# Kernel tuning notes

Hardware: AMD Instinct MI355X
Metric: run time of the kernel (lower is better)

## Reference

```python
import jax, jax.numpy as jnp
import numpy as np

B, DIN, DOUT = 16, 64, 64
P1_, P2_, P3_ = 64, 32, 16
BN_EPS = 1e-5


def setup_inputs() -> dict:
    key = jax.random.key(0)
    ks = jax.random.split(key, 8)
    A = jax.random.normal(ks[0], (B, DIN, P1_, P2_, P3_), dtype=jnp.float32)
    ini_p = float(np.sqrt(3.0 / DOUT / DIN))
    ini_qk = float(np.sqrt(1.0 / DOUT / DIN))
    def uni(k, s):
        return jax.random.uniform(k, (DOUT, DIN), dtype=jnp.float32, minval=-s, maxval=s)
    return {
        "A": A,
        "P1": uni(ks[1], ini_p),
        "P2": uni(ks[2], ini_p),
        "P3": uni(ks[3], ini_p),
        "P4": uni(ks[4], ini_p),
        "q": uni(ks[5], ini_qk),
        "k": uni(ks[6], ini_qk),
        "gamma": jnp.ones((DOUT,), jnp.float32),
        "beta": jnp.zeros((DOUT,), jnp.float32),
        "permutation_size1": P1_,
        "permutation_size2": P2_,
        "permutation_size3": P3_,
        "BATCH_SIZE": B,
    }


def reference(A, P1, P2, P3, P4, q, k, gamma, beta,
              permutation_size1, permutation_size2, permutation_size3, BATCH_SIZE):
    b = BATCH_SIZE
    dout = P1.shape[0]
    p1, p2, p3 = permutation_size1, permutation_size2, permutation_size3
    # branch 1: full per-element channel mix  [B, dout, p1, p2, p3]
    A1 = jnp.einsum('oi,bixyz->boxyz', P1, A)
    # branch 2: mean over p3, project, broadcast over p3
    A2 = jnp.einsum('oi,bixy->boxy', P2, A.mean(-1))[..., None]
    # branch 3: mean over p2, project, broadcast over p2
    A3 = jnp.einsum('oi,bixz->boxz', P3, A.mean(-2))[:, :, :, None, :]
    # attention over p1 with flattened (p2*p3) as the contraction axis
    Q = jnp.einsum('oi,bixyz->boxyz', q, A).reshape(b, dout, p1, p2 * p3)
    K = jnp.einsum('oi,bixyz->boxyz', k, A).reshape(b, dout, p1, p2 * p3)
    Alpha = jnp.einsum('bcxm,bcym->bcxy', Q, K)  # [B, dout, p1, p1]
    Alpha_norm = jnp.abs(Alpha) / jnp.linalg.norm(Alpha, axis=3, keepdims=True)
    V = jnp.einsum('oi,bixyz->boxyz', P4, A).reshape(b, dout, p1, p2 * p3)
    Y = jnp.einsum('bcxy,bcym->bcxm', Alpha_norm, V).reshape(b, dout, p1, p2, p3)
    out = A1 + 0.1 * A2 + 0.1 * A3 + 0.1 * Y
    out = jax.nn.relu(out)
    # BatchNorm3d (training-mode batch statistics, biased variance)
    mean = out.mean(axis=(0, 2, 3, 4), keepdims=True)
    var = out.var(axis=(0, 2, 3, 4), keepdims=True)
    out = (out - mean) * jax.lax.rsqrt(var + BN_EPS)
    out = out * gamma[None, :, None, None, None] + beta[None, :, None, None, None]
    return out
```

## Files before the change

### kernel.cpp

```cpp
#include <hip/hip_runtime.h>

typedef __attribute__((ext_vector_type(8))) short short8;
typedef __attribute__((ext_vector_type(4))) float f32x4;
typedef __attribute__((ext_vector_type(8))) unsigned short u16x8;
typedef __attribute__((ext_vector_type(4))) unsigned short u16x4;
typedef __attribute__((ext_vector_type(4))) unsigned int u32x4;
typedef unsigned short u16;

#define DEVINL __device__ __forceinline__

DEVINL u16 f2bf(float f) {
  unsigned u = __builtin_bit_cast(unsigned, f);
  unsigned r = (u + 0x7fffu + ((u >> 16) & 1u)) >> 16;
  return (u16)r;
}
DEVINL float bf2f(u16 h) {
  unsigned u = ((unsigned)h) << 16;
  return __builtin_bit_cast(float, u);
}
DEVINL unsigned pk2(float a, float b) {
  return (unsigned)f2bf(a) | ((unsigned)f2bf(b) << 16);
}
DEVINL int swzc(int row, int chunk) { return chunk ^ ((row ^ (row >> 3)) & 7); }
DEVINL int tile_byte(int row, int chunk) { return row * 128 + swzc(row, chunk) * 16; }

__global__ void kw_convert(const float* __restrict__ P1, const float* __restrict__ q,
                           const float* __restrict__ k, const float* __restrict__ P4,
                           const float* __restrict__ P2, const float* __restrict__ P3,
                           u16* __restrict__ Wbf) {
  int t = threadIdx.x;
  const float* srcs[6] = {P1, q, k, P4, P2, P3};
  for (int w = 0; w < 6; ++w)
    for (int e = t; e < 4096; e += 256) Wbf[w * 4096 + e] = f2bf(srcs[w][e]);
}

__global__ __launch_bounds__(512, 4) void k_projA(
    const float* __restrict__ A, const u16* __restrict__ Wbf, u16* __restrict__ A1,
    u16* __restrict__ Q, u16* __restrict__ Km, u16* __restrict__ V,
    float* __restrict__ A2g, float* __restrict__ A3g, int g0) {
  __shared__ __align__(16) u16 tile[512 * 64];
  __shared__ __align__(16) u16 meanT[48 * 64];
  const int t = threadIdx.x;
  const int w = t >> 6, l = t & 63;
  const int lr = l & 15, lh = l >> 4;
  const int x = blockIdx.x, bg = blockIdx.y;
  const long bglob = g0 + bg;

  {
    const int s4 = t & 31, i4 = t >> 5;
    const float* ap = A + (bglob * 64 + i4 * 4) * 32768 + (long)x * 512 + s4 * 4;
#pragma unroll
    for (int si = 0; si < 4; ++si) {
      f32x4 v0 = *(const f32x4*)(ap + si * 128);
      f32x4 v1 = *(const f32x4*)(ap + si * 128 + 32768);
      f32x4 v2 = *(const f32x4*)(ap + si * 128 + 65536);
      f32x4 v3 = *(const f32x4*)(ap + si * 128 + 98304);
#pragma unroll
      for (int e = 0; e < 4; ++e) {
        int s = si * 128 + s4 * 4 + e;
        u16x4 pk = {f2bf(v0[e]), f2bf(v1[e]), f2bf(v2[e]), f2bf(v3[e])};
        *(u16x4*)((char*)tile + tile_byte(s, i4 >> 1) + (i4 & 1) * 8) = pk;
      }
    }
  }
  __syncthreads();

  {
    const int ic = t & 7, zh = (t >> 3) & 1, y = t >> 4;
    float acc[8] = {0, 0, 0, 0, 0, 0, 0, 0};
#pragma unroll
    for (int zz = 0; zz < 8; ++zz) {
      int row = y * 16 + zh * 8 + zz;
      u16x8 v = *(const u16x8*)((const char*)tile + tile_byte(row, ic));
#pragma unroll
      for (int e = 0; e < 8; ++e) acc[e] += bf2f(v[e]);
    }
#pragma unroll
    for (int e = 0; e < 8; ++e) acc[e] += __shfl_xor(acc[e], 8);
    if (zh == 0) {
      u16x8 pk;
#pragma unroll
      for (int e = 0; e < 8; ++e) pk[e] = f2bf(acc[e] * (1.0f / 16.0f));
      *(u16x8*)((char*)meanT + tile_byte(y, ic)) = pk;
    }
  }
  {
    const int ic = t & 7, yg = (t >> 3) & 3, z = t >> 5;
    float acc[8] = {0, 0, 0, 0, 0, 0, 0, 0};
#pragma unroll
    for (int yy = 0; yy < 8; ++yy) {
      int row = (yg * 8 + yy) * 16 + z;
      u16x8 v = *(const u16x8*)((const char*)tile + tile_byte(row, ic));
#pragma unroll
      for (int e = 0; e < 8; ++e) acc[e] += bf2f(v[e]);
    }
#pragma unroll
    for (int e = 0; e < 8; ++e) {
      acc[e] += __shfl_xor(acc[e], 8);
      acc[e] += __shfl_xor(acc[e], 16);
    }
    if (yg == 0) {
      u16x8 pk;
#pragma unroll
      for (int e = 0; e < 8; ++e) pk[e] = f2bf(acc[e] * (1.0f / 32.0f));
      *(u16x8*)((char*)meanT + tile_byte(32 + z, ic)) = pk;
    }
  }
  __syncthreads();

  if (w < 3) {
    const int ct = w;
    const u16* wb2 = Wbf + (w == 2 ? 5 : 4) * 4096;
    const int colrow = (w == 2) ? 32 + lr : ct * 16 + lr;
    f32x4 acc2[4];
#pragma unroll
    for (int ot = 0; ot < 4; ++ot) acc2[ot] = {0.0f, 0.0f, 0.0f, 0.0f};
#pragma unroll
    for (int ks = 0; ks < 2; ++ks) {
      short8 mf = *(const short8*)((const char*)meanT + tile_byte(colrow, ks * 4 + lh));
#pragma unroll
      for (int ot = 0; ot < 4; ++ot) {
        short8 w2f = *(const short8*)(wb2 + (ot * 16 + lr) * 64 + ks * 32 + lh * 8);
        acc2[ot] = __builtin_amdgcn_mfma_f32_16x16x32_bf16(w2f, mf, acc2[ot], 0, 0, 0);
      }
    }
#pragma unroll
    for (int ot = 0; ot < 4; ++ot)
#pragma unroll
      for (int r = 0; r < 4; ++r) {
        int o = ot * 16 + lh * 4 + r;
        if (w < 2)
          A2g[(((long)bg * 64 + o) * 64 + x) * 32 + ct * 16 + lr] = acc2[ot][r];
        else
          A3g[(((long)bg * 64 + o) * 64 + x) * 16 + lr] = acc2[ot][r];
      }
  }

  const int m = w & 3, sh = w >> 2;
  const u16* wb = Wbf + m * 4096;
  short8 wf[4][2];
#pragma unroll
  for (int ot = 0; ot < 4; ++ot)
#pragma unroll
    for (int ks = 0; ks < 2; ++ks)
      wf[ot][ks] = *(const short8*)(wb + (ot * 16 + lr) * 64 + ks * 32 + lh * 8);
  u16* outp = (m == 0) ? A1 : (m == 1) ? Q : (m == 2) ? Km : V;
  outp += (long)bg * 64 * 32768;
  const int odd = lh & 1;
  const int p8 = (lh >> 1) * 8;

  for (int stp = 0; stp < 8; ++stp) {
    const int srowE = sh * 256 + stp * 32 + lr;
    const int srowO = srowE + 16;
    short8 aE0 = *(const short8*)((const char*)tile + tile_byte(srowE, lh));
    short8 aE1 = *(const short8*)((const char*)tile + tile_byte(srowE, 4 + lh));
    short8 aO0 = *(const short8*)((const char*)tile + tile_byte(srowO, lh));
    short8 aO1 = *(const short8*)((const char*)tile + tile_byte(srowO, 4 + lh));
    const int sbase = x * 512 + sh * 256 + stp * 32 + odd * 16 + p8;
#pragma unroll
    for (int ot = 0; ot < 4; ++ot) {
      f32x4 accE = {0.0f, 0.0f, 0.0f, 0.0f}, accO = {0.0f, 0.0f, 0.0f, 0.0f};
      accE = __builtin_amdgcn_mfma_f32_16x16x32_bf16(aE0, wf[ot][0], accE, 0, 0, 0);
      accE = __builtin_amdgcn_mfma_f32_16x16x32_bf16(aE1, wf[ot][1], accE, 0, 0, 0);
      accO = __builtin_amdgcn_mfma_f32_16x16x32_bf16(aO0, wf[ot][0], accO, 0, 0, 0);
      accO = __builtin_amdgcn_mfma_f32_16x16x32_bf16(aO1, wf[ot][1], accO, 0, 0, 0);
      unsigned pE0 = pk2(accE[0], accE[1]), pE1 = pk2(accE[2], accE[3]);
      unsigned pO0 = pk2(accO[0], accO[1]), pO1 = pk2(accO[2], accO[3]);
      unsigned rE0 = __shfl_xor((int)pE0, 16), rE1 = __shfl_xor((int)pE1, 16);
      unsigned rO0 = __shfl_xor((int)pO0, 16), rO1 = __shfl_xor((int)pO1, 16);
      u32x4 sv;
      if (odd) sv = (u32x4){rO0, rO1, pO0, pO1};
      else     sv = (u32x4){pE0, pE1, rE0, rE1};
      *(u32x4*)(outp + (long)(ot * 16 + lr) * 32768 + sbase) = sv;
    }
  }
}

__global__ __launch_bounds__(256) void k_attn(const u16* __restrict__ Qg,
                                              const u16* __restrict__ Kg,
                                              const u16* __restrict__ Vg,
                                              const u16* __restrict__ A1g,
                                              const float* __restrict__ A2g,
                                              const float* __restrict__ A3g,
                                              float* __restrict__ out,
                                              float* __restrict__ partials, int g0) {
  __shared__ __align__(16) u16 Qc[4096], Kc[4096], Vt[4096], An[4096];
  __shared__ float red[8];
  const int t = threadIdx.x, w = t >> 6, l = t & 63;
  const int lr = l & 15, lh = l >> 4;
  const int c = blockIdx.x, bg = blockIdx.y;
  const long bglob = g0 + bg;
  const long base = ((long)bg * 64 + c) * 32768;
  const u16* Qp = Qg + base;
  const u16* Kp = Kg + base;
  const u16* Vp = Vg + base;
  const u16* A1p = A1g + base;

  f32x4 accA[4];
#pragma unroll
  for (int yt = 0; yt < 4; ++yt) accA[yt] = {0.0f, 0.0f, 0.0f, 0.0f};

  const int srow = t >> 3, scc = t & 7;
  for (int mc = 0; mc < 8; ++mc) {
#pragma unroll
    for (int it = 0; it < 2; ++it) {
      int row = srow + it * 32;
      int gch = scc ^ ((row ^ (row >> 3)) & 7);
      u16x8 qv = *(const u16x8*)(Qp + row * 512 + mc * 64 + gch * 8);
      u16x8 kv = *(const u16x8*)(Kp + row * 512 + mc * 64 + gch * 8);
      *(u16x8*)((char*)Qc + row * 128 + scc * 16) = qv;
      *(u16x8*)((char*)Kc + row * 128 + scc * 16) = kv;
    }
    __syncthreads();
    short8 qf[2];
#pragma unroll
    for (int ks = 0; ks < 2; ++ks)
      qf[ks] = *(const short8*)((const char*)Qc + tile_byte(16 * w + lr, ks * 4 + lh));
#pragma unroll
    for (int ks = 0; ks < 2; ++ks)
#pragma unroll
      for (int yt = 0; yt < 4; ++yt) {
        short8 kf = *(const short8*)((const char*)Kc + tile_byte(yt * 16 + lr, ks * 4 + lh));
        accA[yt] = __builtin_amdgcn_mfma_f32_16x16x32_bf16(qf[ks], kf, accA[yt], 0, 0, 0);
      }
    __syncthreads();
  }

  float rsq[4];
#pragma unroll
  for (int r = 0; r < 4; ++r) {
    float s = 0.0f;
#pragma unroll
    for (int yt = 0; yt < 4; ++yt) s += accA[yt][r] * accA[yt][r];
#pragma unroll
    for (int msk = 1; msk < 16; msk <<= 1) s += __shfl_xor(s, msk);
    rsq[r] = rsqrtf(s);
  }
#pragma unroll
  for (int yt = 0; yt < 4; ++yt)
#pragma unroll
    for (int r = 0; r < 4; ++r) {
      int xr = 16 * w + 4 * lh + r;
      int y = yt * 16 + lr;
      *(u16*)((char*)An + xr * 128 + swzc(xr, y >> 3) * 16 + (y & 7) * 2) =
          f2bf(fabsf(accA[yt][r]) * rsq[r]);
    }

  float ls = 0.0f, lsq = 0.0f;
  const float* A2p = A2g + ((long)bg * 64 + c) * 2048;
  const float* A3p = A3g + ((long)bg * 64 + c) * 1024;
  float* outp = out + (bglob * 64 + c) * 32768;
  const int m4 = t & 15, y4 = t >> 4;
  const int x = 16 * w + lr;

  for (int mc = 0; mc < 8; ++mc) {
    __syncthreads();
    u16x4 vr[4];
#pragma unroll
    for (int r = 0; r < 4; ++r)
      vr[r] = *(const u16x4*)(Vp + (y4 * 4 + r) * 512 + mc * 64 + m4 * 4);
#pragma unroll
    for (int ci = 0; ci < 4; ++ci) {
      int mrow = m4 * 4 + ci;
      u16x4 pk = {vr[0][ci], vr[1][ci], vr[2][ci], vr[3][ci]};
      *(u16x4*)((char*)Vt + tile_byte(mrow, y4 >> 1) + (y4 & 1) * 8) = pk;
    }
    __syncthreads();

    f32x4 accY[4];
#pragma unroll
    for (int mt = 0; mt < 4; ++mt) accY[mt] = {0.0f, 0.0f, 0.0f, 0.0f};
#pragma unroll
    for (int ks = 0; ks < 2; ++ks) {
      short8 anf = *(const short8*)((const char*)An + tile_byte(16 * w + lr, ks * 4 + lh));
#pragma unroll
      for (int mt = 0; mt < 4; ++mt) {
        short8 vf = *(const short8*)((const char*)Vt + tile_byte(mt * 16 + lr, ks * 4 + lh));
        accY[mt] = __builtin_amdgcn_mfma_f32_16x16x32_bf16(vf, anf, accY[mt], 0, 0, 0);
      }
    }
    f32x4 a3v = *(const f32x4*)(A3p + x * 16 + lh * 4);
#pragma unroll
    for (int mt = 0; mt < 4; ++mt) {
      float a2v = A2p[x * 32 + mc * 4 + mt];
      int mbase = mc * 64 + mt * 16 + lh * 4;
      u16x4 a1v = *(const u16x4*)(A1p + x * 512 + mbase);
      f32x4 o;
#pragma unroll
      for (int r = 0; r < 4; ++r) {
        float val = bf2f(a1v[r]) + 0.1f * (a2v + a3v[r] + accY[mt][r]);
        val = fmaxf(val, 0.0f);
        o[r] = val;
        ls += val;
        lsq += val * val;
      }
      *(f32x4*)(outp + x * 512 + mbase) = o;
    }
  }

#pragma unroll
  for (int off = 32; off > 0; off >>= 1) {
    ls += __shfl_xor(ls, off);
    lsq += __shfl_xor(lsq, off);
  }
  if (l == 0) {
    red[w] = ls;
    red[4 + w] = lsq;
  }
  __syncthreads();
  if (t == 0) {
    partials[2 * (bglob * 64 + c) + 0] = red[0] + red[1] + red[2] + red[3];
    partials[2 * (bglob * 64 + c) + 1] = red[4] + red[5] + red[6] + red[7];
  }
}

__global__ void k_stats(const float* __restrict__ partials, const float* __restrict__ gamma,
                        const float* __restrict__ beta, float* __restrict__ sb) {
  int c = threadIdx.x;
  if (c >= 64) return;
  float S = 0.0f, SQ = 0.0f;
  for (int b = 0; b < 16; ++b) {
    S += partials[2 * (b * 64 + c) + 0];
    SQ += partials[2 * (b * 64 + c) + 1];
  }
  const float N = 524288.0f;
  float mean = S / N;
  float var = SQ / N - mean * mean;
  float rs = rsqrtf(var + 1e-5f);
  float scale = gamma[c] * rs;
  sb[c] = scale;
  sb[64 + c] = beta[c] - mean * scale;
}

__global__ void k_bn(float* __restrict__ out, const float* __restrict__ sb) {
  long idx = ((long)blockIdx.x * 256 + threadIdx.x) * 4;
  int c = (int)((idx >> 15) & 63);
  float scale = sb[c], bias = sb[64 + c];
  f32x4 v = *(f32x4*)(out + idx);
#pragma unroll
  for (int r = 0; r < 4; ++r) v[r] = v[r] * scale + bias;
  *(f32x4*)(out + idx) = v;
}

extern "C" void kernel_launch(void* const* d_in, const int* in_sizes, int n_in, void* d_out,
                              int out_size, void* d_ws, size_t ws_size, hipStream_t stream) {
  (void)in_sizes; (void)n_in; (void)out_size;
  const float* A = (const float*)d_in[0];
  const float* P1 = (const float*)d_in[1];
  const float* P2 = (const float*)d_in[2];
  const float* P3 = (const float*)d_in[3];
  const float* P4 = (const float*)d_in[4];
  const float* q = (const float*)d_in[5];
  const float* k = (const float*)d_in[6];
  const float* gamma = (const float*)d_in[7];
  const float* beta = (const float*)d_in[8];
  float* out = (float*)d_out;
  char* ws = (char*)d_ws;

  u16* Wbf = (u16*)ws;
  float* partials = (float*)(ws + 49152);
  float* sb = (float*)(ws + 57344);
  const size_t GR = 65536;
  const size_t SZ_M = (size_t)64 * 32768 * 2;
  const size_t SZ_A2 = (size_t)64 * 64 * 32 * 4;
  const size_t SZ_A3 = (size_t)64 * 64 * 16 * 4;
  const size_t perb = 4 * SZ_M + SZ_A2 + SZ_A3;
  int G = 1;
  if (ws_size > GR + perb) G = (int)((ws_size - GR) / perb);
  if (G > 16) G = 16;
  if (G < 1) G = 1;

  u16* A1 = (u16*)(ws + GR);
  u16* Qw = (u16*)(ws + GR + (size_t)G * SZ_M);
  u16* Kw = (u16*)(ws + GR + (size_t)G * SZ_M * 2);
  u16* Vw = (u16*)(ws + GR + (size_t)G * SZ_M * 3);
  float* A2 = (float*)(ws + GR + (size_t)G * SZ_M * 4);
  float* A3 = (float*)((char*)A2 + (size_t)G * SZ_A2);

  kw_convert<<<1, 256, 0, stream>>>(P1, q, k, P4, P2, P3, Wbf);
  for (int g0 = 0; g0 < 16; g0 += G) {
    int Gc = (16 - g0) < G ? (16 - g0) : G;
    k_projA<<<dim3(64, Gc), 512, 0, stream>>>(A, Wbf, A1, Qw, Kw, Vw, A2, A3, g0);
    k_attn<<<dim3(64, Gc), 256, 0, stream>>>(Qw, Kw, Vw, A1, A2, A3, out, partials, g0);
  }
  k_stats<<<1, 64, 0, stream>>>(partials, gamma, beta, sb);
  k_bn<<<32768, 256, 0, stream>>>(out, sb);
}
```

Baseline: 271.1 us.

## Halve projA LDS tile in two passes and stage pre-BN output in bf16

k_projA now processes its 512-position slab in two halves through a 256-row LDS tile, so it can request higher occupancy (launch bounds 8). The p3-mean is computed per half and the p2-mean is accumulated across both halves. k_attn writes the pre-BatchNorm activations as bf16 into a workspace buffer, and k_bn reads that bf16 buffer and writes fp32 output. This replaces the fp32 write plus fp32 read-modify-write of the output, cutting intermediate traffic. The cost is bf16 rounding before normalization and a large extra workspace allocation, which can shrink the group count G.

```diff
diff --git a/kernel.cpp b/kernel.cpp
--- a/kernel.cpp
+++ b/kernel.cpp
@@ -34,11 +34,11 @@
     for (int e = t; e < 4096; e += 256) Wbf[w * 4096 + e] = f2bf(srcs[w][e]);
 }
 
-__global__ __launch_bounds__(512, 4) void k_projA(
+__global__ __launch_bounds__(512, 8) void k_projA(
     const float* __restrict__ A, const u16* __restrict__ Wbf, u16* __restrict__ A1,
     u16* __restrict__ Q, u16* __restrict__ Km, u16* __restrict__ V,
     float* __restrict__ A2g, float* __restrict__ A3g, int g0) {
-  __shared__ __align__(16) u16 tile[512 * 64];
+  __shared__ __align__(16) u16 tile[256 * 64];
   __shared__ __align__(16) u16 meanT[48 * 64];
   const int t = threadIdx.x;
   const int w = t >> 6, l = t & 63;
@@ -46,64 +46,114 @@
   const int x = blockIdx.x, bg = blockIdx.y;
   const long bglob = g0 + bg;
 
+  const int m = w & 3, sh = w >> 2;
+  const u16* wb = Wbf + m * 4096;
+  short8 wf[4][2];
+#pragma unroll
+  for (int ot = 0; ot < 4; ++ot)
+#pragma unroll
+    for (int ks = 0; ks < 2; ++ks)
+      wf[ot][ks] = *(const short8*)(wb + (ot * 16 + lr) * 64 + ks * 32 + lh * 8);
+  u16* outp = (m == 0) ? A1 : (m == 1) ? Q : (m == 2) ? Km : V;
+  outp += (long)bg * 64 * 32768;
+  const int odd = lh & 1;
+  const int p8 = (lh >> 1) * 8;
+
+  const int icM = t & 7, ygM = (t >> 3) & 3, zM = t >> 5;
+  float m2acc[8] = {0, 0, 0, 0, 0, 0, 0, 0};
+
+  for (int h = 0; h < 2; ++h) {
+    {
+      const int s4 = t & 31, i4 = t >> 5;
+      const float* ap =
+          A + (bglob * 64 + i4 * 4) * 32768 + (long)x * 512 + h * 256 + s4 * 4;
+#pragma unroll
+      for (int si = 0; si < 2; ++si) {
+        f32x4 v0 = *(const f32x4*)(ap + si * 128);
+        f32x4 v1 = *(const f32x4*)(ap + si * 128 + 32768);
+        f32x4 v2 = *(const f32x4*)(ap + si * 128 + 65536);
+        f32x4 v3 = *(const f32x4*)(ap + si * 128 + 98304);
+#pragma unroll
+        for (int e = 0; e < 4; ++e) {
+          int s = si * 128 + s4 * 4 + e;
+          u16x4 pk = {f2bf(v0[e]), f2bf(v1[e]), f2bf(v2[e]), f2bf(v3[e])};
+          *(u16x4*)((char*)tile + tile_byte(s, i4 >> 1) + (i4 & 1) * 8) = pk;
+        }
+      }
+    }
+    __syncthreads();
+
+    {
+      const int ic = t & 7, zq = (t >> 3) & 3, y16 = t >> 5;
+      float acc[8] = {0, 0, 0, 0, 0, 0, 0, 0};
+#pragma unroll
+      for (int zz = 0; zz < 4; ++zz) {
+        int row = y16 * 16 + zq * 4 + zz;
+        u16x8 v = *(const u16x8*)((const char*)tile + tile_byte(row, ic));
+#pragma unroll
+        for (int e = 0; e < 8; ++e) acc[e] += bf2f(v[e]);
+      }
+#pragma unroll
+      for (int e = 0; e < 8; ++e) {
+        acc[e] += __shfl_xor(acc[e], 8);
+        acc[e] += __shfl_xor(acc[e], 16);
+      }
+      if (zq == 0) {
+        u16x8 pk;
+#pragma unroll
+        for (int e = 0; e < 8; ++e) pk[e] = f2bf(acc[e] * (1.0f / 16.0f));
+        *(u16x8*)((char*)meanT + tile_byte(h * 16 + y16, ic)) = pk;
+      }
+    }
+    {
+#pragma unroll
+      for (int yy = 0; yy < 4; ++yy) {
+        int row = (ygM * 4 + yy) * 16 + zM;
+        u16x8 v = *(const u16x8*)((const char*)tile + tile_byte(row, icM));
+#pragma unroll
+        for (int e = 0; e < 8; ++e) m2acc[e] += bf2f(v[e]);
+      }
+    }
+
+    for (int stp = 0; stp < 4; ++stp) {
+      const int srowE = sh * 128 + stp * 32 + lr;
+      const int srowO = srowE + 16;
+      short8 aE0 = *(const short8*)((const char*)tile + tile_byte(srowE, lh));
+      short8 aE1 = *(const short8*)((const char*)tile + tile_byte(srowE, 4 + lh));
+      short8 aO0 = *(const short8*)((const char*)tile + tile_byte(srowO, lh));
+      short8 aO1 = *(const short8*)((const char*)tile + tile_byte(srowO, 4 + lh));
+      const int sbase = x * 512 + h * 256 + sh * 128 + stp * 32 + odd * 16 + p8;
+#pragma unroll
+      for (int ot = 0; ot < 4; ++ot) {
+        f32x4 accE = {0.0f, 0.0f, 0.0f, 0.0f}, accO = {0.0f, 0.0f, 0.0f, 0.0f};
+        accE = __builtin_amdgcn_mfma_f32_16x16x32_bf16(aE0, wf[ot][0], accE, 0, 0, 0);
+        accE = __builtin_amdgcn_mfma_f32_16x16x32_bf16(aE1, wf[ot][1], accE, 0, 0, 0);
+        accO = __builtin_amdgcn_mfma_f32_16x16x32_bf16(aO0, wf[ot][0], accO, 0, 0, 0);
+        accO = __builtin_amdgcn_mfma_f32_16x16x32_bf16(aO1, wf[ot][1], accO, 0, 0, 0);
+        unsigned pE0 = pk2(accE[0], accE[1]), pE1 = pk2(accE[2], accE[3]);
+        unsigned pO0 = pk2(accO[0], accO[1]), pO1 = pk2(accO[2], accO[3]);
+        unsigned rE0 = __shfl_xor((int)pE0, 16), rE1 = __shfl_xor((int)pE1, 16);
+        unsigned rO0 = __shfl_xor((int)pO0, 16), rO1 = __shfl_xor((int)pO1, 16);
+        u32x4 sv;
+        if (odd) sv = (u32x4){rO0, rO1, pO0, pO1};
+        else     sv = (u32x4){pE0, pE1, rE0, rE1};
+        *(u32x4*)(outp + (long)(ot * 16 + lr) * 32768 + sbase) = sv;
+      }
+    }
+    __syncthreads();
+  }
+
   {
-    const int s4 = t & 31, i4 = t >> 5;
-    const float* ap = A + (bglob * 64 + i4 * 4) * 32768 + (long)x * 512 + s4 * 4;
-#pragma unroll
-    for (int si = 0; si < 4; ++si) {
-      f32x4 v0 = *(const f32x4*)(ap + si * 128);
-      f32x4 v1 = *(const f32x4*)(ap + si * 128 + 32768);
-      f32x4 v2 = *(const f32x4*)(ap + si * 128 + 65536);
-      f32x4 v3 = *(const f32x4*)(ap + si * 128 + 98304);
-#pragma unroll
-      for (int e = 0; e < 4; ++e) {
-        int s = si * 128 + s4 * 4 + e;
-        u16x4 pk = {f2bf(v0[e]), f2bf(v1[e]), f2bf(v2[e]), f2bf(v3[e])};
-        *(u16x4*)((char*)tile + tile_byte(s, i4 >> 1) + (i4 & 1) * 8) = pk;
-      }
-    }
-  }
-  __syncthreads();
-
-  {
-    const int ic = t & 7, zh = (t >> 3) & 1, y = t >> 4;
-    float acc[8] = {0, 0, 0, 0, 0, 0, 0, 0};
-#pragma unroll
-    for (int zz = 0; zz < 8; ++zz) {
-      int row = y * 16 + zh * 8 + zz;
-      u16x8 v = *(const u16x8*)((const char*)tile + tile_byte(row, ic));
-#pragma unroll
-      for (int e = 0; e < 8; ++e) acc[e] += bf2f(v[e]);
-    }
-#pragma unroll
-    for (int e = 0; e < 8; ++e) acc[e] += __shfl_xor(acc[e], 8);
-    if (zh == 0) {
+#pragma unroll
+    for (int e = 0; e < 8; ++e) {
+      m2acc[e] += __shfl_xor(m2acc[e], 8);
+      m2acc[e] += __shfl_xor(m2acc[e], 16);
+    }
+    if (ygM == 0) {
       u16x8 pk;
 #pragma unroll
-      for (int e = 0; e < 8; ++e) pk[e] = f2bf(acc[e] * (1.0f / 16.0f));
-      *(u16x8*)((char*)meanT + tile_byte(y, ic)) = pk;
-    }
-  }
-  {
-    const int ic = t & 7, yg = (t >> 3) & 3, z = t >> 5;
-    float acc[8] = {0, 0, 0, 0, 0, 0, 0, 0};
-#pragma unroll
-    for (int yy = 0; yy < 8; ++yy) {
-      int row = (yg * 8 + yy) * 16 + z;
-      u16x8 v = *(const u16x8*)((const char*)tile + tile_byte(row, ic));
-#pragma unroll
-      for (int e = 0; e < 8; ++e) acc[e] += bf2f(v[e]);
-    }
-#pragma unroll
-    for (int e = 0; e < 8; ++e) {
-      acc[e] += __shfl_xor(acc[e], 8);
-      acc[e] += __shfl_xor(acc[e], 16);
-    }
-    if (yg == 0) {
-      u16x8 pk;
-#pragma unroll
-      for (int e = 0; e < 8; ++e) pk[e] = f2bf(acc[e] * (1.0f / 32.0f));
-      *(u16x8*)((char*)meanT + tile_byte(32 + z, ic)) = pk;
+      for (int e = 0; e < 8; ++e) pk[e] = f2bf(m2acc[e] * (1.0f / 32.0f));
+      *(u16x8*)((char*)meanT + tile_byte(32 + zM, icM)) = pk;
     }
   }
   __syncthreads();
@@ -135,45 +185,6 @@
           A3g[(((long)bg * 64 + o) * 64 + x) * 16 + lr] = acc2[ot][r];
       }
   }
-
-  const int m = w & 3, sh = w >> 2;
-  const u16* wb = Wbf + m * 4096;
-  short8 wf[4][2];
-#pragma unroll
-  for (int ot = 0; ot < 4; ++ot)
-#pragma unroll
-    for (int ks = 0; ks < 2; ++ks)
-      wf[ot][ks] = *(const short8*)(wb + (ot * 16 + lr) * 64 + ks * 32 + lh * 8);
-  u16* outp = (m == 0) ? A1 : (m == 1) ? Q : (m == 2) ? Km : V;
-  outp += (long)bg * 64 * 32768;
-  const int odd = lh & 1;
-  const int p8 = (lh >> 1) * 8;
-
-  for (int stp = 0; stp < 8; ++stp) {
-    const int srowE = sh * 256 + stp * 32 + lr;
-    const int srowO = srowE + 16;
-    short8 aE0 = *(const short8*)((const char*)tile + tile_byte(srowE, lh));
-    short8 aE1 = *(const short8*)((const char*)tile + tile_byte(srowE, 4 + lh));
-    short8 aO0 = *(const short8*)((const char*)tile + tile_byte(srowO, lh));
-    short8 aO1 = *(const short8*)((const char*)tile + tile_byte(srowO, 4 + lh));
-    const int sbase = x * 512 + sh * 256 + stp * 32 + odd * 16 + p8;
-#pragma unroll
-    for (int ot = 0; ot < 4; ++ot) {
-      f32x4 accE = {0.0f, 0.0f, 0.0f, 0.0f}, accO = {0.0f, 0.0f, 0.0f, 0.0f};
-      accE = __builtin_amdgcn_mfma_f32_16x16x32_bf16(aE0, wf[ot][0], accE, 0, 0, 0);
-      accE = __builtin_amdgcn_mfma_f32_16x16x32_bf16(aE1, wf[ot][1], accE, 0, 0, 0);
-      accO = __builtin_amdgcn_mfma_f32_16x16x32_bf16(aO0, wf[ot][0], accO, 0, 0, 0);
-      accO = __builtin_amdgcn_mfma_f32_16x16x32_bf16(aO1, wf[ot][1], accO, 0, 0, 0);
-      unsigned pE0 = pk2(accE[0], accE[1]), pE1 = pk2(accE[2], accE[3]);
-      unsigned pO0 = pk2(accO[0], accO[1]), pO1 = pk2(accO[2], accO[3]);
-      unsigned rE0 = __shfl_xor((int)pE0, 16), rE1 = __shfl_xor((int)pE1, 16);
-      unsigned rO0 = __shfl_xor((int)pO0, 16), rO1 = __shfl_xor((int)pO1, 16);
-      u32x4 sv;
-      if (odd) sv = (u32x4){rO0, rO1, pO0, pO1};
-      else     sv = (u32x4){pE0, pE1, rE0, rE1};
-      *(u32x4*)(outp + (long)(ot * 16 + lr) * 32768 + sbase) = sv;
-    }
-  }
 }
 
 __global__ __launch_bounds__(256) void k_attn(const u16* __restrict__ Qg,
@@ -182,7 +193,7 @@
                                               const u16* __restrict__ A1g,
                                               const float* __restrict__ A2g,
                                               const float* __restrict__ A3g,
-                                              float* __restrict__ out,
+                                              u16* __restrict__ outbf,
                                               float* __restrict__ partials, int g0) {
   __shared__ __align__(16) u16 Qc[4096], Kc[4096], Vt[4096], An[4096];
   __shared__ float red[8];
@@ -249,7 +260,7 @@
   float ls = 0.0f, lsq = 0.0f;
   const float* A2p = A2g + ((long)bg * 64 + c) * 2048;
   const float* A3p = A3g + ((long)bg * 64 + c) * 1024;
-  float* outp = out + (bglob * 64 + c) * 32768;
+  u16* outp = outbf + (bglob * 64 + c) * 32768;
   const int m4 = t & 15, y4 = t >> 4;
   const int x = 16 * w + lr;
 
@@ -285,16 +296,16 @@
       float a2v = A2p[x * 32 + mc * 4 + mt];
       int mbase = mc * 64 + mt * 16 + lh * 4;
       u16x4 a1v = *(const u16x4*)(A1p + x * 512 + mbase);
-      f32x4 o;
+      u16x4 o;
 #pragma unroll
       for (int r = 0; r < 4; ++r) {
         float val = bf2f(a1v[r]) + 0.1f * (a2v + a3v[r] + accY[mt][r]);
         val = fmaxf(val, 0.0f);
-        o[r] = val;
+        o[r] = f2bf(val);
         ls += val;
         lsq += val * val;
       }
-      *(f32x4*)(outp + x * 512 + mbase) = o;
+      *(u16x4*)(outp + x * 512 + mbase) = o;
     }
   }
 
@@ -332,14 +343,20 @@
   sb[64 + c] = beta[c] - mean * scale;
 }
 
-__global__ void k_bn(float* __restrict__ out, const float* __restrict__ sb) {
-  long idx = ((long)blockIdx.x * 256 + threadIdx.x) * 4;
+__global__ void k_bn(const u16* __restrict__ outbf, float* __restrict__ out,
+                     const float* __restrict__ sb) {
+  long idx = ((long)blockIdx.x * 256 + threadIdx.x) * 8;
   int c = (int)((idx >> 15) & 63);
   float scale = sb[c], bias = sb[64 + c];
-  f32x4 v = *(f32x4*)(out + idx);
-#pragma unroll
-  for (int r = 0; r < 4; ++r) v[r] = v[r] * scale + bias;
-  *(f32x4*)(out + idx) = v;
+  u16x8 v = *(const u16x8*)(outbf + idx);
+  f32x4 o0, o1;
+#pragma unroll
+  for (int r = 0; r < 4; ++r) {
+    o0[r] = bf2f(v[r]) * scale + bias;
+    o1[r] = bf2f(v[4 + r]) * scale + bias;
+  }
+  *(f32x4*)(out + idx) = o0;
+  *(f32x4*)(out + idx + 4) = o1;
 }
 
 extern "C" void kernel_launch(void* const* d_in, const int* in_sizes, int n_in, void* d_out,
@@ -361,28 +378,31 @@
   float* partials = (float*)(ws + 49152);
   float* sb = (float*)(ws + 57344);
   const size_t GR = 65536;
+  const size_t OUTBF = (size_t)16 * 64 * 32768 * 2;
+  u16* outbf = (u16*)(ws + GR);
   const size_t SZ_M = (size_t)64 * 32768 * 2;
   const size_t SZ_A2 = (size_t)64 * 64 * 32 * 4;
   const size_t SZ_A3 = (size_t)64 * 64 * 16 * 4;
   const size_t perb = 4 * SZ_M + SZ_A2 + SZ_A3;
+  const size_t base0 = GR + OUTBF;
   int G = 1;
-  if (ws_size > GR + perb) G = (int)((ws_size - GR) / perb);
+  if (ws_size > base0 + perb) G = (int)((ws_size - base0) / perb);
   if (G > 16) G = 16;
   if (G < 1) G = 1;
 
-  u16* A1 = (u16*)(ws + GR);
-  u16* Qw = (u16*)(ws + GR + (size_t)G * SZ_M);
-  u16* Kw = (u16*)(ws + GR + (size_t)G * SZ_M * 2);
-  u16* Vw = (u16*)(ws + GR + (size_t)G * SZ_M * 3);
-  float* A2 = (float*)(ws + GR + (size_t)G * SZ_M * 4);
+  u16* A1 = (u16*)(ws + base0);
+  u16* Qw = (u16*)(ws + base0 + (size_t)G * SZ_M);
+  u16* Kw = (u16*)(ws + base0 + (size_t)G * SZ_M * 2);
+  u16* Vw = (u16*)(ws + base0 + (size_t)G * SZ_M * 3);
+  float* A2 = (float*)(ws + base0 + (size_t)G * SZ_M * 4);
   float* A3 = (float*)((char*)A2 + (size_t)G * SZ_A2);
 
   kw_convert<<<1, 256, 0, stream>>>(P1, q, k, P4, P2, P3, Wbf);
   for (int g0 = 0; g0 < 16; g0 += G) {
     int Gc = (16 - g0) < G ? (16 - g0) : G;
     k_projA<<<dim3(64, Gc), 512, 0, stream>>>(A, Wbf, A1, Qw, Kw, Vw, A2, A3, g0);
-    k_attn<<<dim3(64, Gc), 256, 0, stream>>>(Qw, Kw, Vw, A1, A2, A3, out, partials, g0);
+    k_attn<<<dim3(64, Gc), 256, 0, stream>>>(Qw, Kw, Vw, A1, A2, A3, outbf, partials, g0);
   }
   k_stats<<<1, 64, 0, stream>>>(partials, gamma, beta, sb);
-  k_bn<<<32768, 256, 0, stream>>>(out, sb);
-}
+  k_bn<<<16384, 256, 0, stream>>>(outbf, out, sb);
+}
```

Result: slower. 416.7 us (+53.7%).
